# Kernel tuning notes

Hardware: AMD Instinct MI355X
Metric: run time of the kernel (lower is better)

## Reference

```python
import jax, jax.numpy as jnp
import numpy as np
from math import comb

DEGREE = 10          # spline degree -> K = DEGREE+1 coefficients per pair
D = 12               # number_variables
N = 1_000_000        # sample size
SPAN = 0.1           # span_factor
# pair ordering: var_num outer loop, covar_num inner ascending -> tril row-major order
VI, CI = np.tril_indices(D, -1)
BINOM = jnp.asarray([comb(DEGREE, k) for k in range(DEGREE + 1)], dtype=jnp.float32)


def setup_inputs() -> dict:
    key = jax.random.key(0)
    k1, k2 = jax.random.split(key)
    inp = jax.random.normal(k1, (N, D), dtype=jnp.float32) * 3.0
    n_pairs = D * (D - 1) // 2  # 66
    # module inits params to 0.1 everywhere; add small noise for a non-degenerate test
    params = 0.1 + 0.05 * jax.random.normal(k2, (DEGREE + 1, n_pairs), dtype=jnp.float32)
    polynomial_range = jnp.stack([jnp.full((D,), -15.0, jnp.float32),
                                  jnp.full((D,), 15.0, jnp.float32)])
    return {"input": inp, "params": params, "polynomial_range": polynomial_range}


def _bernstein_basis(x):
    # x: [N, D] scaled to ~[0,1]; returns [N, D, K]
    i = jnp.arange(DEGREE + 1, dtype=x.dtype)
    xx = x[..., None]
    return BINOM * xx ** i * (1.0 - xx) ** (DEGREE - i)


def reference(input, params, polynomial_range):
    # inflate the polynomial range by span_factor, then scale each column to [0,1]
    low, high = polynomial_range[0], polynomial_range[1]
    width = high - low
    lo = low - SPAN * width
    hi = high + SPAN * width
    x = (input - lo) / (hi - lo)                    # [N, D]
    basis = _bernstein_basis(x)                     # [N, D, K]
    # scatter per-pair coefficients into a strictly-lower-triangular [K, D, D] tensor;
    # P[:, v, c] = params[:, pair_index(v, c)], zero elsewhere
    P = jnp.zeros((DEGREE + 1, D, D), params.dtype).at[:, VI, CI].set(params)
    # forward pass: output[n, v] = input[n, v] + sum_{c<v} lambda_{v,c}(input[n, c]) * input[n, c]
    # note lambda is multiplied by input[:, c] and lambda = basis @ coeffs, so we can fold
    # input[:, c] into the contraction only after computing lambda; here lambda*input is
    # einsum over k then elementwise — fuse: first lambda matrix entries, then weight.
    lam = jnp.einsum('nck,kvc->nvc', basis, P)      # [N, D, D] strictly lower lambda entries
    return input + jnp.einsum('nvc,nc->nv', lam, input)
```

## Files before the change

kernel.cpp:

```cpp
#include <hip/hip_runtime.h>

#define DV    12
#define NP    66
#define KK    11
#define NFEAT 121
#define KPAD  128

#define WS_SA 1024
#define WS_SB 1036

typedef __attribute__((ext_vector_type(8))) short bf16x8;
typedef __attribute__((ext_vector_type(4))) float f32x4;

__device__ __constant__ float c_binom[KK] =
    {1.f, 10.f, 45.f, 120.f, 210.f, 252.f, 210.f, 120.f, 45.f, 10.f, 1.f};

__device__ __forceinline__ unsigned bfb(float f) {
    union { float f; unsigned u; } c; c.f = f;
    return (c.u + 0x7FFFu + ((c.u >> 16) & 1u)) >> 16;
}

__global__ __launch_bounds__(256)
void prep_kernel(const float* __restrict__ params,
                 const float* __restrict__ pr,
                 void* __restrict__ wsv)
{
    unsigned short* w2 = (unsigned short*)wsv;
    float* wsf = (float*)wsv;
    const int tid = threadIdx.x;
    for (int i = tid; i < 16 * KPAD; i += 256) {
        const int v  = i >> 7;
        const int kk = i & 127;
        float val = 0.0f;
        if (v < DV && kk < NFEAT) {
            const int c = kk / KK;
            const int k = kk - c * KK;
            if (c < v) {
                const int p = v * (v - 1) / 2 + c;
                val = params[k * NP + p] * c_binom[k];
            }
        }
        w2[i] = (unsigned short)bfb(val);
    }
    if (tid < DV) {
        float low  = pr[tid];
        float high = pr[DV + tid];
        float w    = high - low;
        float lo   = low - 0.1f * w;
        float hi   = high + 0.1f * w;
        float inv  = 1.0f / (hi - lo);
        wsf[WS_SA + tid] = inv;
        wsf[WS_SB + tid] = -lo * inv;
    }
}

__global__ __launch_bounds__(64)
void decor_mfma(const float* __restrict__ in,
                const void* __restrict__ wsv,
                float* __restrict__ out,
                int n)
{
    __shared__ __align__(16) char lds[64 * 256];

    const int l = threadIdx.x;
    const int q = l >> 4;
    const int p = l & 15;
    const long s0 = (long)blockIdx.x * 64;
    const unsigned swz = (unsigned)((l & 7) << 4);

    const float* wsf = (const float*)wsv;
    const char*  w2b = (const char*)wsv;

    bf16x8 af[4];
#pragma unroll
    for (int s = 0; s < 4; ++s) {
        union { int4 i; bf16x8 h; } u;
        u.i = *(const int4*)(w2b + p * 256 + s * 64 + q * 16);
        af[s] = u.h;
    }

    f32x4 acc[4];
#pragma unroll
    for (int g = 0; g < 4; ++g) {
        const long sg = s0 + 16 * g + p;
        float4 cin = make_float4(0.f, 0.f, 0.f, 0.f);
        if (q < 3 && sg < n) cin = *(const float4*)(in + sg * 12 + q * 4);
        acc[g][0] = cin.x; acc[g][1] = cin.y; acc[g][2] = cin.z; acc[g][3] = cin.w;
    }

    const long mys = s0 + l;
    float x[DV];
    {
        float4 r0 = make_float4(0.f,0.f,0.f,0.f), r1 = r0, r2 = r0;
        if (mys < n) {
            const float4* in4 = (const float4*)(in + mys * 12);
            r0 = in4[0]; r1 = in4[1]; r2 = in4[2];
        }
        x[0]=r0.x; x[1]=r0.y; x[2] =r0.z; x[3] =r0.w;
        x[4]=r1.x; x[5]=r1.y; x[6] =r1.z; x[7] =r1.w;
        x[8]=r2.x; x[9]=r2.y; x[10]=r2.z; x[11]=r2.w;
    }

    unsigned uw[64];
#pragma unroll
    for (int c = 0; c < KK; ++c) {
        const float t  = __builtin_fmaf(x[c], wsf[WS_SA + c], wsf[WS_SB + c]);
        const float u1 = 1.0f - t;
        float tp[KK];
        tp[0] = 1.0f;
#pragma unroll
        for (int k = 1; k < KK; ++k) tp[k] = tp[k - 1] * t;
        float gl[KK];
        gl[KK - 1] = x[c];
#pragma unroll
        for (int k = KK - 2; k >= 0; --k) gl[k] = gl[k + 1] * u1;
        float fl[KK];
        fl[0] = gl[0];
#pragma unroll
        for (int k = 1; k < KK; ++k) fl[k] = tp[k] * gl[k];

#pragma unroll
        for (int k = 0; k < KK; ++k) {
            const int idx = c * KK + k;
            const unsigned b = bfb(fl[k]);
            if ((idx & 1) == 0) uw[idx >> 1] = b;
            else                uw[idx >> 1] |= (b << 16);
            if ((idx & 7) == 7) {
                const int grp = idx >> 3;
                int4 w4 = make_int4(uw[grp*4], uw[grp*4+1], uw[grp*4+2], uw[grp*4+3]);
                *(int4*)(lds + (unsigned)l * 256u + (((unsigned)grp * 16u) ^ swz)) = w4;
            }
        }
    }
    uw[60] &= 0xFFFFu;
    uw[61] = 0u; uw[62] = 0u; uw[63] = 0u;
    *(int4*)(lds + (unsigned)l * 256u + ((15u * 16u) ^ swz)) =
        make_int4(uw[60], uw[61], uw[62], uw[63]);

    __syncthreads();

#pragma unroll
    for (int g = 0; g < 4; ++g) {
        const unsigned row = (unsigned)(16 * g + p);
#pragma unroll
        for (int s = 0; s < 4; ++s) {
            union { int4 i; bf16x8 h; } u;
            u.i = *(const int4*)(lds + row * 256u +
                                 (((unsigned)(s * 64 + q * 16)) ^ swz));
            acc[g] = __builtin_amdgcn_mfma_f32_16x16x32_bf16(af[s], u.h, acc[g], 0, 0, 0);
        }
    }

#pragma unroll
    for (int g = 0; g < 4; ++g) {
        const long sg = s0 + 16 * g + p;
        if (q < 3 && sg < n) {
            float4 o = make_float4(acc[g][0], acc[g][1], acc[g][2], acc[g][3]);
            *(float4*)(out + sg * 12 + q * 4) = o;
        }
    }
}

extern "C" void kernel_launch(void* const* d_in, const int* in_sizes, int n_in,
                              void* d_out, int out_size, void* d_ws, size_t ws_size,
                              hipStream_t stream)
{
    const float* in     = (const float*)d_in[0];
    const float* params = (const float*)d_in[1];
    const float* pr     = (const float*)d_in[2];
    float* out          = (float*)d_out;

    const int n = in_sizes[0] / DV;

    prep_kernel<<<1, 256, 0, stream>>>(params, pr, d_ws);
    const int grid = (n + 63) / 64;
    decor_mfma<<<grid, 64, 0, stream>>>(in, d_ws, (float*)d_out, n);
}
```

Before: 119.6 us.

## Use 256-thread blocks and split basis staging into two half-size LDS phases

Each block now runs four waves, each owning a 64-row tile, instead of one wave per block. Each wave's LDS staging buffer is halved by computing the first six covariates' Bernstein features, running the first two MFMA K-steps, then reusing the buffer for the remaining features and K-steps. The aim is to raise occupancy and cut LDS footprint, at the cost of extra block-wide barriers between phases.

```diff
diff --git a/kernel.cpp b/kernel.cpp
--- a/kernel.cpp
+++ b/kernel.cpp
@@ -3,8 +3,6 @@
 #define DV    12
 #define NP    66
 #define KK    11
-#define NFEAT 121
-#define KPAD  128
 
 #define WS_SA 1024
 #define WS_SB 1036
@@ -28,11 +26,11 @@
     unsigned short* w2 = (unsigned short*)wsv;
     float* wsf = (float*)wsv;
     const int tid = threadIdx.x;
-    for (int i = tid; i < 16 * KPAD; i += 256) {
+    for (int i = tid; i < 16 * 128; i += 256) {
         const int v  = i >> 7;
         const int kk = i & 127;
         float val = 0.0f;
-        if (v < DV && kk < NFEAT) {
+        if (v < DV && kk < 121) {
             const int c = kk / KK;
             const int k = kk - c * KK;
             if (c < v) {
@@ -54,18 +52,22 @@
     }
 }
 
-__global__ __launch_bounds__(64)
+__global__ __launch_bounds__(256, 4)
 void decor_mfma(const float* __restrict__ in,
                 const void* __restrict__ wsv,
                 float* __restrict__ out,
                 int n)
 {
-    __shared__ __align__(16) char lds[64 * 256];
-
-    const int l = threadIdx.x;
+    __shared__ __align__(16) char lds_all[4][64 * 128];
+
+    const int tid = threadIdx.x;
+    const int wv  = tid >> 6;
+    const int l   = tid & 63;
+    char* lds = lds_all[wv];
+
     const int q = l >> 4;
     const int p = l & 15;
-    const long s0 = (long)blockIdx.x * 64;
+    const long s0 = (long)blockIdx.x * 256 + (long)wv * 64;
     const unsigned swz = (unsigned)((l & 7) << 4);
 
     const float* wsf = (const float*)wsv;
@@ -102,16 +104,19 @@
     }
 
     unsigned uw[64];
-#pragma unroll
-    for (int c = 0; c < KK; ++c) {
-        const float t  = __builtin_fmaf(x[c], wsf[WS_SA + c], wsf[WS_SB + c]);
+    float pend = 0.0f;
+
+#pragma unroll
+    for (int c = 0; c < 6; ++c) {
+        const float xc = x[c];
+        const float t  = __builtin_fmaf(xc, wsf[WS_SA + c], wsf[WS_SB + c]);
         const float u1 = 1.0f - t;
         float tp[KK];
         tp[0] = 1.0f;
 #pragma unroll
         for (int k = 1; k < KK; ++k) tp[k] = tp[k - 1] * t;
         float gl[KK];
-        gl[KK - 1] = x[c];
+        gl[KK - 1] = xc;
 #pragma unroll
         for (int k = KK - 2; k >= 0; --k) gl[k] = gl[k + 1] * u1;
         float fl[KK];
@@ -121,21 +126,19 @@
 
 #pragma unroll
         for (int k = 0; k < KK; ++k) {
-            const int idx = c * KK + k;
-            const unsigned b = bfb(fl[k]);
-            if ((idx & 1) == 0) uw[idx >> 1] = b;
-            else                uw[idx >> 1] |= (b << 16);
-            if ((idx & 7) == 7) {
-                const int grp = idx >> 3;
-                int4 w4 = make_int4(uw[grp*4], uw[grp*4+1], uw[grp*4+2], uw[grp*4+3]);
-                *(int4*)(lds + (unsigned)l * 256u + (((unsigned)grp * 16u) ^ swz)) = w4;
+            const int gidx = c * KK + k;
+            if ((gidx & 1) == 0) pend = fl[k];
+            else {
+                uw[gidx >> 1] = bfb(pend) | (bfb(fl[k]) << 16);
+                if ((gidx & 7) == 7) {
+                    const int grp = gidx >> 3;
+                    *(int4*)(lds + (unsigned)l * 128u +
+                             ((((unsigned)(grp & 7)) * 16u) ^ swz)) =
+                        make_int4(uw[grp*4], uw[grp*4+1], uw[grp*4+2], uw[grp*4+3]);
+                }
             }
         }
     }
-    uw[60] &= 0xFFFFu;
-    uw[61] = 0u; uw[62] = 0u; uw[63] = 0u;
-    *(int4*)(lds + (unsigned)l * 256u + ((15u * 16u) ^ swz)) =
-        make_int4(uw[60], uw[61], uw[62], uw[63]);
 
     __syncthreads();
 
@@ -143,10 +146,63 @@
     for (int g = 0; g < 4; ++g) {
         const unsigned row = (unsigned)(16 * g + p);
 #pragma unroll
-        for (int s = 0; s < 4; ++s) {
+        for (int s = 0; s < 2; ++s) {
             union { int4 i; bf16x8 h; } u;
-            u.i = *(const int4*)(lds + row * 256u +
+            u.i = *(const int4*)(lds + row * 128u +
                                  (((unsigned)(s * 64 + q * 16)) ^ swz));
+            acc[g] = __builtin_amdgcn_mfma_f32_16x16x32_bf16(af[s], u.h, acc[g], 0, 0, 0);
+        }
+    }
+
+    __syncthreads();
+
+#pragma unroll
+    for (int c = 6; c < KK; ++c) {
+        const float xc = x[c];
+        const float t  = __builtin_fmaf(xc, wsf[WS_SA + c], wsf[WS_SB + c]);
+        const float u1 = 1.0f - t;
+        float tp[KK];
+        tp[0] = 1.0f;
+#pragma unroll
+        for (int k = 1; k < KK; ++k) tp[k] = tp[k - 1] * t;
+        float gl[KK];
+        gl[KK - 1] = xc;
+#pragma unroll
+        for (int k = KK - 2; k >= 0; --k) gl[k] = gl[k + 1] * u1;
+        float fl[KK];
+        fl[0] = gl[0];
+#pragma unroll
+        for (int k = 1; k < KK; ++k) fl[k] = tp[k] * gl[k];
+
+#pragma unroll
+        for (int k = 0; k < KK; ++k) {
+            const int gidx = c * KK + k;
+            if ((gidx & 1) == 0) pend = fl[k];
+            else {
+                uw[gidx >> 1] = bfb(pend) | (bfb(fl[k]) << 16);
+                if ((gidx & 7) == 7) {
+                    const int grp = gidx >> 3;
+                    *(int4*)(lds + (unsigned)l * 128u +
+                             ((((unsigned)(grp & 7)) * 16u) ^ swz)) =
+                        make_int4(uw[grp*4], uw[grp*4+1], uw[grp*4+2], uw[grp*4+3]);
+                }
+            }
+        }
+    }
+    uw[60] = bfb(pend);
+    *(int4*)(lds + (unsigned)l * 128u + ((7u * 16u) ^ swz)) =
+        make_int4(uw[60], 0, 0, 0);
+
+    __syncthreads();
+
+#pragma unroll
+    for (int g = 0; g < 4; ++g) {
+        const unsigned row = (unsigned)(16 * g + p);
+#pragma unroll
+        for (int s = 2; s < 4; ++s) {
+            union { int4 i; bf16x8 h; } u;
+            u.i = *(const int4*)(lds + row * 128u +
+                                 (((unsigned)((s - 2) * 64 + q * 16)) ^ swz));
             acc[g] = __builtin_amdgcn_mfma_f32_16x16x32_bf16(af[s], u.h, acc[g], 0, 0, 0);
         }
     }
@@ -173,6 +229,6 @@
     const int n = in_sizes[0] / DV;
 
     prep_kernel<<<1, 256, 0, stream>>>(params, pr, d_ws);
-    const int grid = (n + 63) / 64;
-    decor_mfma<<<grid, 64, 0, stream>>>(in, d_ws, (float*)d_out, n);
-}
+    const int grid = (n + 255) / 256;
+    decor_mfma<<<grid, 256, 0, stream>>>(in, d_ws, out, n);
+}
```

After: 113.8 us. 1.05x faster.
